# Performance work log

Measured on AMD Instinct MI355X. Metric: run time of the kernel, lower is better.

The kernel has to match this reference:

```python
import jax, jax.numpy as jnp
import numpy as np

B, S, D, H = 2, 2048, 1024, 16
DH = D // H  # key_dim = embed_dim // num_heads
NEG = 1e9    # Keras masked-softmax adder magnitude
EPS = 1e-6


def setup_inputs() -> dict:
    key = jax.random.key(0)
    ks = jax.random.split(key, 6)
    sc = 1.0 / np.sqrt(D)
    return {
        "x": jax.random.normal(ks[0], (B, S, D), jnp.float32),
        "Wq": jax.random.normal(ks[1], (D, H, DH), jnp.float32) * sc,
        "bq": jnp.zeros((H, DH), jnp.float32),
        "Wk": jax.random.normal(ks[2], (D, H, DH), jnp.float32) * sc,
        "bk": jnp.zeros((H, DH), jnp.float32),
        "Wv": jax.random.normal(ks[3], (D, H, DH), jnp.float32) * sc,
        "bv": jnp.zeros((H, DH), jnp.float32),
        "Wo": jax.random.normal(ks[4], (H, DH, D), jnp.float32) * (1.0 / np.sqrt(D)),
        "bo": jnp.zeros((D,), jnp.float32),
        "gamma": jnp.ones((D,), jnp.float32),
        "beta": jnp.zeros((D,), jnp.float32),
    }


def reference(x, Wq, bq, Wk, bk, Wv, bv, Wo, bo, gamma, beta):
    # Keras MultiHeadAttention(query=x, value=x), inference (dropouts are identity)
    q = jnp.einsum("bsd,dhk->bshk", x, Wq) + bq  # [B,S,H,DH]
    k = jnp.einsum("bsd,dhk->bshk", x, Wk) + bk
    v = jnp.einsum("bsd,dhk->bshk", x, Wv) + bv

    scores = jnp.einsum("bqhd,bkhd->bhqk", q, k) / jnp.sqrt(jnp.asarray(DH, x.dtype))
    # Source: mask = 1 - band_part(ones, -1, 0) -> ones strictly ABOVE diagonal.
    # Keras attends where mask==1 and adds (1-mask)*(-1e9) elsewhere. Faithful:
    i = jnp.arange(S)[:, None]
    j = jnp.arange(S)[None, :]
    allowed = (j > i).astype(scores.dtype)  # [S,S], strict upper triangle
    scores = scores + (allowed - 1.0) * NEG  # subtract 1e9 where not allowed
    probs = jax.nn.softmax(scores, axis=-1)

    ctx = jnp.einsum("bhqk,bkhd->bqhd", probs, v)  # [B,S,H,DH]
    attn_out = jnp.einsum("bqhd,hdo->bqo", ctx, Wo) + bo  # [B,S,D]

    # residual + LayerNorm(eps=1e-6)
    y = x + attn_out
    mu = jnp.mean(y, axis=-1, keepdims=True)
    var = jnp.mean(jnp.square(y - mu), axis=-1, keepdims=True)
    return (y - mu) * jax.lax.rsqrt(var + EPS) * gamma + beta
```

## Files before the change

kernel.cpp:

```cpp
#include <hip/hip_runtime.h>
#include <hip/hip_bf16.h>

typedef __hip_bfloat16 bf16;
typedef __attribute__((ext_vector_type(8))) short bf16x8;
typedef __attribute__((ext_vector_type(4))) float f32x4;

constexpr int Bc  = 2;
constexpr int Sc  = 2048;
constexpr int Dc  = 1024;
constexpr int Hc  = 16;
constexpr int DHc = 64;
constexpr int BS  = Bc * Sc;
constexpr int NT  = Sc / 64;

__device__ __forceinline__ float bs2f(unsigned short u) {
    union { unsigned int i; float f; } v; v.i = ((unsigned int)u) << 16; return v.f;
}
__device__ __forceinline__ short f2bs(float x) {
    bf16 h = __float2bfloat16(x);
    return *reinterpret_cast<short*>(&h);
}

typedef const __attribute__((address_space(1))) unsigned int* as1_u32p;
typedef __attribute__((address_space(3))) unsigned int* as3_u32p;
__device__ __forceinline__ void gl_lds16(const void* g, void* l) {
    __builtin_amdgcn_global_load_lds((as1_u32p)g, (as3_u32p)l, 16, 0, 0);
}

__global__ __launch_bounds__(256) void cast_x(const float* __restrict__ in,
                                              short* __restrict__ out) {
    const int i = (blockIdx.x * 256 + threadIdx.x) * 4;
    const float4 v = *(const float4*)(in + i);
    ushort4 o;
    o.x = (unsigned short)f2bs(v.x);
    o.y = (unsigned short)f2bs(v.y);
    o.z = (unsigned short)f2bs(v.z);
    o.w = (unsigned short)f2bs(v.w);
    *(ushort4*)(out + i) = o;
}

__global__ __launch_bounds__(256) void transpose_cast(
    const float* __restrict__ w0, const float* __restrict__ w1,
    const float* __restrict__ w2, const float* __restrict__ w3,
    short* __restrict__ outbase)
{
    __shared__ float T[64][65];
    const int z = blockIdx.z;
    const float* in = (z == 0) ? w0 : (z == 1) ? w1 : (z == 2) ? w2 : w3;
    short* out = outbase + (size_t)z * 1024 * 1024;
    const int k0 = blockIdx.x * 64, n0 = blockIdx.y * 64;
    const int t = threadIdx.x;
    #pragma unroll
    for (int it = 0; it < 4; ++it) {
        const int s = it * 256 + t;
        const int r = s >> 4, c = (s & 15) * 4;
        *(float4*)&T[r][c] = *(const float4*)(in + (size_t)(k0 + r) * 1024 + n0 + c);
    }
    __syncthreads();
    #pragma unroll
    for (int it = 0; it < 4; ++it) {
        const int s = it * 256 + t;
        const int rr = s >> 4, cc = (s & 15) * 4;
        ushort4 o;
        o.x = (unsigned short)f2bs(T[cc + 0][rr]);
        o.y = (unsigned short)f2bs(T[cc + 1][rr]);
        o.z = (unsigned short)f2bs(T[cc + 2][rr]);
        o.w = (unsigned short)f2bs(T[cc + 3][rr]);
        *(ushort4*)(out + (size_t)(n0 + rr) * 1024 + k0 + cc) = o;
    }
}

__global__ __launch_bounds__(256, 3) void gemm_bt(
    const short* __restrict__ A, const short* __restrict__ BTbase,
    const float* __restrict__ b0, const float* __restrict__ b1,
    const float* __restrict__ b2, short* __restrict__ Cbase)
{
    __shared__ __align__(16) short As[128 * 64];
    __shared__ __align__(16) short Bs[128 * 64];

    const int z = blockIdx.z;
    const short* BT = BTbase + (size_t)z * 1024 * 1024;
    const float* bias = (z == 0) ? b0 : (z == 1) ? b1 : b2;
    short* C = Cbase + (size_t)z * BS * Dc;

    const int t = threadIdx.x;
    const int lane = t & 63, w = t >> 6;
    const int quad = lane >> 4, l16 = lane & 15;
    const int wm = (w & 1) * 64, wn = (w >> 1) * 64;
    const int row0 = blockIdx.y * 128;
    const int col0 = blockIdx.x * 128;
    const int sw = l16 & 7;

    f32x4 acc[4][4] = {};

    for (int kt = 0; kt < 1024; kt += 64) {
        __syncthreads();
        #pragma unroll
        for (int i = 0; i < 4; ++i) {
            const int f = i * 256 + t;
            const int r = f >> 3;
            const int g = (f & 7) ^ (r & 7);
            short* lb = &As[(i * 256 + w * 64) * 8];
            gl_lds16(A + (size_t)(row0 + r) * 1024 + kt + g * 8, lb);
            short* lb2 = &Bs[(i * 256 + w * 64) * 8];
            gl_lds16(BT + (size_t)(col0 + r) * 1024 + kt + g * 8, lb2);
        }
        __syncthreads();
        #pragma unroll
        for (int ks = 0; ks < 2; ++ks) {
            bf16x8 av[4], bv[4];
            #pragma unroll
            for (int mt = 0; mt < 4; ++mt) {
                const int r = wm + mt * 16 + l16;
                av[mt] = *(const bf16x8*)&As[r * 64 + ((ks * 4 + quad) ^ sw) * 8];
            }
            #pragma unroll
            for (int nt = 0; nt < 4; ++nt) {
                const int r = wn + nt * 16 + l16;
                bv[nt] = *(const bf16x8*)&Bs[r * 64 + ((ks * 4 + quad) ^ sw) * 8];
            }
            #pragma unroll
            for (int mt = 0; mt < 4; ++mt)
                #pragma unroll
                for (int nt = 0; nt < 4; ++nt)
                    acc[mt][nt] = __builtin_amdgcn_mfma_f32_16x16x32_bf16(
                        av[mt], bv[nt], acc[mt][nt], 0, 0, 0);
        }
    }

    float bvv[4];
    #pragma unroll
    for (int nt = 0; nt < 4; ++nt) bvv[nt] = bias[col0 + wn + nt * 16 + l16];
    #pragma unroll
    for (int mt = 0; mt < 4; ++mt)
        #pragma unroll
        for (int reg = 0; reg < 4; ++reg) {
            const size_t row = row0 + wm + mt * 16 + quad * 4 + reg;
            #pragma unroll
            for (int nt = 0; nt < 4; ++nt) {
                const int col = col0 + wn + nt * 16 + l16;
                C[row * 1024 + col] = f2bs(acc[mt][nt][reg] + bvv[nt]);
            }
        }
}

__device__ __forceinline__ int psw_off(int row, int col) {
    return row * 72 + (row >> 2) * 48 + col;
}

template<bool DIAG>
__device__ __forceinline__ void qtile_step(
    const bf16x8 (&qf)[2],
    const short (&Ks)[64][72], const short (&VsT)[64][72],
    short* __restrict__ Psw,
    const int k0, const int row_base,
    const int quad, const int l16,
    float (&l)[4], f32x4 (&O)[4])
{
    bf16x8 kf[2][4];
    #pragma unroll
    for (int ks = 0; ks < 2; ++ks)
        #pragma unroll
        for (int nt = 0; nt < 4; ++nt)
            kf[ks][nt] = *(const bf16x8*)&Ks[nt * 16 + l16][ks * 32 + quad * 8];

    f32x4 S[4] = {};
    #pragma unroll
    for (int ks = 0; ks < 2; ++ks)
        #pragma unroll
        for (int nt = 0; nt < 4; ++nt)
            S[nt] = __builtin_amdgcn_mfma_f32_16x16x32_bf16(qf[ks], kf[ks][nt], S[nt], 0, 0, 0);

    #pragma unroll
    for (int nt = 0; nt < 4; ++nt) {
        #pragma unroll
        for (int reg = 0; reg < 4; ++reg) {
            float s = fminf(S[nt][reg] * 0.125f, 80.f);
            if (DIAG) {
                const int col = k0 + nt * 16 + l16;
                const int row = row_base + quad * 4 + reg;
                s = (col > row) ? s : -87.0f;
            }
            const float p = __expf(s);
            S[nt][reg] = p;
            l[reg] += p;
        }
    }

    #pragma unroll
    for (int nt = 0; nt < 4; ++nt)
        #pragma unroll
        for (int reg = 0; reg < 4; ++reg)
            Psw[psw_off(quad * 4 + reg, nt * 16 + l16)] = f2bs(S[nt][reg]);

    #pragma unroll
    for (int ks = 0; ks < 2; ++ks) {
        const bf16x8 pf = *(const bf16x8*)&Psw[psw_off(l16, ks * 32 + quad * 8)];
        #pragma unroll
        for (int nt = 0; nt < 4; ++nt) {
            const bf16x8 vf = *(const bf16x8*)&VsT[nt * 16 + l16][ks * 32 + quad * 8];
            O[nt] = __builtin_amdgcn_mfma_f32_16x16x32_bf16(pf, vf, O[nt], 0, 0, 0);
        }
    }
}

__global__ __launch_bounds__(512, 4) void attn_mfma(
    const short* __restrict__ Qg, const short* __restrict__ Kg,
    const short* __restrict__ Vg, short* __restrict__ CTX)
{
    __shared__ __align__(16) short Ks [2][64][72];
    __shared__ __align__(16) short VsT[2][64][72];
    __shared__ __align__(16) short Ps[8][1296];

    const int tid  = threadIdx.x;
    const int lane = tid & 63, w = tid >> 6;
    const int quad = lane >> 4, l16 = lane & 15;
    const int wq   = w & 3;
    const bool isA = (w < 4);
    const int p  = blockIdx.x;
    const int h  = blockIdx.y;
    const int b  = blockIdx.z;
    const size_t rb = (size_t)b * Sc;
    const int cb = h * DHc;

    const int myT0 = isA ? p : (NT - 1 - p);
    const int q0   = myT0 * 64;

    bf16x8 qf[2];
    {
        const short* qp = Qg + (rb + q0 + wq * 16 + l16) * (size_t)Dc + cb + quad * 8;
        qf[0] = *(const bf16x8*)(qp);
        qf[1] = *(const bf16x8*)(qp + 32);
    }

    float l[4] = {};
    f32x4 O[4] = {};

    const int skey = tid & 63, sseg = (tid >> 6) * 8;

    {
        const int buf = p & 1;
        const size_t g = (rb + p * 64 + skey) * (size_t)Dc + cb + sseg;
        const bf16x8 kv = *(const bf16x8*)(Kg + g);
        const bf16x8 vv = *(const bf16x8*)(Vg + g);
        *(bf16x8*)&Ks[buf][skey][sseg] = kv;
        #pragma unroll
        for (int e = 0; e < 8; ++e) VsT[buf][sseg + e][skey] = vv[e];
    }
    __syncthreads();

    for (int t = p; t < NT; ++t) {
        const int cur = t & 1;
        const bool havenext = (t + 1 < NT);
        bf16x8 pk, pv;
        if (havenext) {
            const size_t g = (rb + (t + 1) * 64 + skey) * (size_t)Dc + cb + sseg;
            pk = *(const bf16x8*)(Kg + g);
            pv = *(const bf16x8*)(Vg + g);
        }

        if (t > myT0) {
            qtile_step<false>(qf, Ks[cur], VsT[cur], Ps[w],
                              t * 64, q0 + wq * 16, quad, l16, l, O);
        } else if (t == myT0) {
            qtile_step<true>(qf, Ks[cur], VsT[cur], Ps[w],
                             t * 64, q0 + wq * 16, quad, l16, l, O);
        }

        if (havenext) {
            *(bf16x8*)&Ks[cur ^ 1][skey][sseg] = pk;
            #pragma unroll
            for (int e = 0; e < 8; ++e) VsT[cur ^ 1][sseg + e][skey] = pv[e];
            __syncthreads();
        }
    }

    #pragma unroll
    for (int off = 1; off < 16; off <<= 1)
        #pragma unroll
        for (int reg = 0; reg < 4; ++reg)
            l[reg] += __shfl_xor(l[reg], off, 64);
    #pragma unroll
    for (int reg = 0; reg < 4; ++reg) l[reg] = 1.0f / l[reg];
    #pragma unroll
    for (int nt = 0; nt < 4; ++nt)
        #pragma unroll
        for (int reg = 0; reg < 4; ++reg) {
            const size_t row = rb + q0 + wq * 16 + quad * 4 + reg;
            CTX[row * Dc + cb + nt * 16 + l16] = f2bs(O[nt][reg] * l[reg]);
        }
}

__global__ __launch_bounds__(256) void vmean(const short* __restrict__ V,
                                             short* __restrict__ CTX)
{
    const int h = blockIdx.x, b = blockIdx.y;
    const int t = threadIdx.x;
    const int dh = t & 63, ck = t >> 6;
    float s = 0.f;
    const short* vp = V + ((size_t)b * Sc + ck * 512) * Dc + h * DHc + dh;
    for (int j = 0; j < 512; ++j) s += bs2f(vp[(size_t)j * Dc]);
    __shared__ float red[4][64];
    red[ck][dh] = s;
    __syncthreads();
    if (ck == 0) {
        const float tot = (red[0][dh] + red[1][dh] + red[2][dh] + red[3][dh]) * (1.f / Sc);
        CTX[((size_t)b * Sc + Sc - 1) * Dc + h * DHc + dh] = f2bs(tot);
    }
}

__global__ __launch_bounds__(256, 4) void resid_ln(
    const float* __restrict__ X, const short* __restrict__ AO,
    const float* __restrict__ gamma, const float* __restrict__ beta,
    float* __restrict__ out)
{
    const int r = blockIdx.x;
    const int t = threadIdx.x;
    const size_t base = (size_t)r * Dc + t * 4;

    const float4 x4 = *(const float4*)(X + base);
    const ushort4 a4 = *(const ushort4*)(AO + base);
    float y[4];
    y[0] = x4.x + bs2f(a4.x);
    y[1] = x4.y + bs2f(a4.y);
    y[2] = x4.z + bs2f(a4.z);
    y[3] = x4.w + bs2f(a4.w);

    float s  = y[0] + y[1] + y[2] + y[3];
    float s2 = y[0]*y[0] + y[1]*y[1] + y[2]*y[2] + y[3]*y[3];
    #pragma unroll
    for (int off = 1; off < 64; off <<= 1) {
        s  += __shfl_xor(s,  off, 64);
        s2 += __shfl_xor(s2, off, 64);
    }
    __shared__ float red[8];
    const int w = t >> 6;
    if ((t & 63) == 0) { red[w] = s; red[4 + w] = s2; }
    __syncthreads();
    s  = red[0] + red[1] + red[2] + red[3];
    s2 = red[4] + red[5] + red[6] + red[7];

    const float mu   = s * (1.0f / Dc);
    const float rstd = rsqrtf(s2 * (1.0f / Dc) - mu * mu + 1e-6f);

    const float4 g4 = *(const float4*)(gamma + t * 4);
    const float4 b4 = *(const float4*)(beta  + t * 4);
    float4 o;
    o.x = (y[0] - mu) * rstd * g4.x + b4.x;
    o.y = (y[1] - mu) * rstd * g4.y + b4.y;
    o.z = (y[2] - mu) * rstd * g4.z + b4.z;
    o.w = (y[3] - mu) * rstd * g4.w + b4.w;
    *(float4*)(out + base) = o;
}

extern "C" void kernel_launch(void* const* d_in, const int* in_sizes, int n_in,
                              void* d_out, int out_size, void* d_ws, size_t ws_size,
                              hipStream_t stream)
{
    (void)in_sizes; (void)n_in; (void)out_size; (void)ws_size;
    const float* x     = (const float*)d_in[0];
    const float* Wq    = (const float*)d_in[1];
    const float* bq    = (const float*)d_in[2];
    const float* Wk    = (const float*)d_in[3];
    const float* bk    = (const float*)d_in[4];
    const float* Wv    = (const float*)d_in[5];
    const float* bv    = (const float*)d_in[6];
    const float* Wo    = (const float*)d_in[7];
    const float* bo    = (const float*)d_in[8];
    const float* gamma = (const float*)d_in[9];
    const float* beta  = (const float*)d_in[10];
    float* out = (float*)d_out;

    const size_t matN = (size_t)BS * Dc;
    const size_t wN   = (size_t)Dc * Dc;
    short* xb = (short*)d_ws;
    short* WT = xb + matN;
    short* Qb = WT + 4 * wN;
    short* Kb = Qb + matN;
    short* Vb = Kb + matN;
    short* Cx = Vb + matN;
    short* AO = Qb;

    cast_x<<<matN / 1024, 256, 0, stream>>>(x, xb);

    dim3 gt(16, 16, 4);
    transpose_cast<<<gt, 256, 0, stream>>>(Wq, Wk, Wv, Wo, WT);

    dim3 gq(Dc / 128, BS / 128, 3);
    gemm_bt<<<gq, 256, 0, stream>>>(xb, WT, bq, bk, bv, Qb);

    dim3 ga(16, Hc, Bc);
    attn_mfma<<<ga, 512, 0, stream>>>(Qb, Kb, Vb, Cx);

    dim3 gv(Hc, Bc);
    vmean<<<gv, 256, 0, stream>>>(Vb, Cx);

    dim3 go(Dc / 128, BS / 128, 1);
    gemm_bt<<<go, 256, 0, stream>>>(Cx, WT + 3 * wN, bo, bo, bo, AO);

    resid_ln<<<BS, 256, 0, stream>>>(x, AO, gamma, beta, out);
}
```

Measured before the change: 222.8 us.

## Run attention blocks with 4 waves processing paired query tiles sequentially

New measurement: 221.6 us. Within noise of the previous version (-0.5%).

```diff
diff --git a/kernel.cpp b/kernel.cpp
--- a/kernel.cpp
+++ b/kernel.cpp
@@ -144,15 +144,12 @@
         }
 }
 
-__device__ __forceinline__ int psw_off(int row, int col) {
-    return row * 72 + (row >> 2) * 48 + col;
-}
 
 template<bool DIAG>
 __device__ __forceinline__ void qtile_step(
     const bf16x8 (&qf)[2],
     const short (&Ks)[64][72], const short (&VsT)[64][72],
-    short* __restrict__ Psw,
+    short (&Psw)[16][72],
     const int k0, const int row_base,
     const int quad, const int l16,
     float (&l)[4], f32x4 (&O)[4])
@@ -175,27 +172,31 @@
     for (int nt = 0; nt < 4; ++nt) {
         #pragma unroll
         for (int reg = 0; reg < 4; ++reg) {
-            float s = fminf(S[nt][reg] * 0.125f, 80.f);
+            float s = fminf(S[nt][reg] * 0.18033688f, 115.4f);
             if (DIAG) {
                 const int col = k0 + nt * 16 + l16;
                 const int row = row_base + quad * 4 + reg;
-                s = (col > row) ? s : -87.0f;
-            }
-            const float p = __expf(s);
+                s = (col > row) ? s : -126.0f;
+            }
+            const float p = exp2f(s);
             S[nt][reg] = p;
             l[reg] += p;
         }
     }
 
     #pragma unroll
-    for (int nt = 0; nt < 4; ++nt)
-        #pragma unroll
-        for (int reg = 0; reg < 4; ++reg)
-            Psw[psw_off(quad * 4 + reg, nt * 16 + l16)] = f2bs(S[nt][reg]);
+    for (int reg = 0; reg < 4; ++reg) {
+        const __hip_bfloat162 lo = __float22bfloat162_rn(make_float2(S[0][reg], S[1][reg]));
+        const __hip_bfloat162 hi = __float22bfloat162_rn(make_float2(S[2][reg], S[3][reg]));
+        uint2 u;
+        u.x = *reinterpret_cast<const unsigned int*>(&lo);
+        u.y = *reinterpret_cast<const unsigned int*>(&hi);
+        *(uint2*)&Psw[quad * 4 + reg][l16 * 4] = u;
+    }
 
     #pragma unroll
     for (int ks = 0; ks < 2; ++ks) {
-        const bf16x8 pf = *(const bf16x8*)&Psw[psw_off(l16, ks * 32 + quad * 8)];
+        const bf16x8 pf = *(const bf16x8*)&Psw[l16][ks * 32 + quad * 8];
         #pragma unroll
         for (int nt = 0; nt < 4; ++nt) {
             const bf16x8 vf = *(const bf16x8*)&VsT[nt * 16 + l16][ks * 32 + quad * 8];
@@ -204,91 +205,107 @@
     }
 }
 
-__global__ __launch_bounds__(512, 4) void attn_mfma(
+__global__ __launch_bounds__(256, 3) void attn_mfma(
     const short* __restrict__ Qg, const short* __restrict__ Kg,
     const short* __restrict__ Vg, short* __restrict__ CTX)
 {
     __shared__ __align__(16) short Ks [2][64][72];
     __shared__ __align__(16) short VsT[2][64][72];
-    __shared__ __align__(16) short Ps[8][1296];
+    __shared__ __align__(16) short Ps[4][16][72];
 
     const int tid  = threadIdx.x;
     const int lane = tid & 63, w = tid >> 6;
     const int quad = lane >> 4, l16 = lane & 15;
-    const int wq   = w & 3;
-    const bool isA = (w < 4);
     const int p  = blockIdx.x;
     const int h  = blockIdx.y;
     const int b  = blockIdx.z;
     const size_t rb = (size_t)b * Sc;
     const int cb = h * DHc;
 
-    const int myT0 = isA ? p : (NT - 1 - p);
-    const int q0   = myT0 * 64;
-
-    bf16x8 qf[2];
-    {
-        const short* qp = Qg + (rb + q0 + wq * 16 + l16) * (size_t)Dc + cb + quad * 8;
-        qf[0] = *(const bf16x8*)(qp);
-        qf[1] = *(const bf16x8*)(qp + 32);
-    }
-
-    float l[4] = {};
-    f32x4 O[4] = {};
-
     const int skey = tid & 63, sseg = (tid >> 6) * 8;
-
-    {
-        const int buf = p & 1;
-        const size_t g = (rb + p * 64 + skey) * (size_t)Dc + cb + sseg;
-        const bf16x8 kv = *(const bf16x8*)(Kg + g);
-        const bf16x8 vv = *(const bf16x8*)(Vg + g);
-        *(bf16x8*)&Ks[buf][skey][sseg] = kv;
-        #pragma unroll
-        for (int e = 0; e < 8; ++e) VsT[buf][sseg + e][skey] = vv[e];
-    }
-    __syncthreads();
-
-    for (int t = p; t < NT; ++t) {
-        const int cur = t & 1;
-        const bool havenext = (t + 1 < NT);
-        bf16x8 pk, pv;
-        if (havenext) {
-            const size_t g = (rb + (t + 1) * 64 + skey) * (size_t)Dc + cb + sseg;
-            pk = *(const bf16x8*)(Kg + g);
-            pv = *(const bf16x8*)(Vg + g);
-        }
-
-        if (t > myT0) {
-            qtile_step<false>(qf, Ks[cur], VsT[cur], Ps[w],
-                              t * 64, q0 + wq * 16, quad, l16, l, O);
-        } else if (t == myT0) {
-            qtile_step<true>(qf, Ks[cur], VsT[cur], Ps[w],
-                             t * 64, q0 + wq * 16, quad, l16, l, O);
-        }
-
-        if (havenext) {
-            *(bf16x8*)&Ks[cur ^ 1][skey][sseg] = pk;
-            #pragma unroll
-            for (int e = 0; e < 8; ++e) VsT[cur ^ 1][sseg + e][skey] = pv[e];
-            __syncthreads();
-        }
-    }
-
-    #pragma unroll
-    for (int off = 1; off < 16; off <<= 1)
-        #pragma unroll
-        for (int reg = 0; reg < 4; ++reg)
-            l[reg] += __shfl_xor(l[reg], off, 64);
-    #pragma unroll
-    for (int reg = 0; reg < 4; ++reg) l[reg] = 1.0f / l[reg];
-    #pragma unroll
-    for (int nt = 0; nt < 4; ++nt)
-        #pragma unroll
-        for (int reg = 0; reg < 4; ++reg) {
-            const size_t row = rb + q0 + wq * 16 + quad * 4 + reg;
-            CTX[row * Dc + cb + nt * 16 + l16] = f2bs(O[nt][reg] * l[reg]);
-        }
+    const int pkey = ((skey & 15) << 2) | (skey >> 4);
+
+    #pragma unroll 1
+    for (int ph = 0; ph < 2; ++ph) {
+        const int myq = ph ? (NT - 1 - p) : p;
+        const int t0  = myq;
+        const int q0  = myq * 64;
+
+        bf16x8 qf[2];
+        {
+            const short* qp = Qg + (rb + q0 + w * 16 + l16) * (size_t)Dc + cb + quad * 8;
+            qf[0] = *(const bf16x8*)(qp);
+            qf[1] = *(const bf16x8*)(qp + 32);
+        }
+        float l[4] = {};
+        f32x4 O[4] = {};
+
+        if (ph) __syncthreads();
+
+        {
+            const int buf = t0 & 1;
+            const size_t g = (rb + t0 * 64 + skey) * (size_t)Dc + cb + sseg;
+            const bf16x8 k0v = *(const bf16x8*)(Kg + g);
+            const bf16x8 k1v = *(const bf16x8*)(Kg + g + 32);
+            const bf16x8 v0v = *(const bf16x8*)(Vg + g);
+            const bf16x8 v1v = *(const bf16x8*)(Vg + g + 32);
+            *(bf16x8*)&Ks[buf][skey][sseg]      = k0v;
+            *(bf16x8*)&Ks[buf][skey][sseg + 32] = k1v;
+            #pragma unroll
+            for (int e = 0; e < 8; ++e) {
+                VsT[buf][sseg + e][pkey]      = v0v[e];
+                VsT[buf][sseg + 32 + e][pkey] = v1v[e];
+            }
+        }
+        __syncthreads();
+
+        for (int t = t0; t < NT; ++t) {
+            const int cur = t & 1;
+            const bool havenext = (t + 1 < NT);
+            bf16x8 pk0, pk1, pv0, pv1;
+            if (havenext) {
+                const size_t g = (rb + (t + 1) * 64 + skey) * (size_t)Dc + cb + sseg;
+                pk0 = *(const bf16x8*)(Kg + g);
+                pk1 = *(const bf16x8*)(Kg + g + 32);
+                pv0 = *(const bf16x8*)(Vg + g);
+                pv1 = *(const bf16x8*)(Vg + g + 32);
+            }
+
+            if (t == t0)
+                qtile_step<true >(qf, Ks[cur], VsT[cur], Ps[w],
+                                  t * 64, q0 + w * 16, quad, l16, l, O);
+            else
+                qtile_step<false>(qf, Ks[cur], VsT[cur], Ps[w],
+                                  t * 64, q0 + w * 16, quad, l16, l, O);
+
+            if (havenext) {
+                const int nb = cur ^ 1;
+                *(bf16x8*)&Ks[nb][skey][sseg]      = pk0;
+                *(bf16x8*)&Ks[nb][skey][sseg + 32] = pk1;
+                #pragma unroll
+                for (int e = 0; e < 8; ++e) {
+                    VsT[nb][sseg + e][pkey]      = pv0[e];
+                    VsT[nb][sseg + 32 + e][pkey] = pv1[e];
+                }
+                __syncthreads();
+            }
+        }
+
+        #pragma unroll
+        for (int off = 1; off < 16; off <<= 1)
+            #pragma unroll
+            for (int reg = 0; reg < 4; ++reg)
+                l[reg] += __shfl_xor(l[reg], off, 64);
+        #pragma unroll
+        for (int reg = 0; reg < 4; ++reg) l[reg] = 1.0f / l[reg];
+        #pragma unroll
+        for (int nt = 0; nt < 4; ++nt)
+            #pragma unroll
+            for (int reg = 0; reg < 4; ++reg) {
+                const size_t row = rb + q0 + w * 16 + quad * 4 + reg;
+                CTX[row * Dc + cb + nt * 16 + l16] = f2bs(O[nt][reg] * l[reg]);
+            }
+    }
 }
 
 __global__ __launch_bounds__(256) void vmean(const short* __restrict__ V,
@@ -390,7 +407,7 @@
     gemm_bt<<<gq, 256, 0, stream>>>(xb, WT, bq, bk, bv, Qb);
 
     dim3 ga(16, Hc, Bc);
-    attn_mfma<<<ga, 512, 0, stream>>>(Qb, Kb, Vb, Cx);
+    attn_mfma<<<ga, 256, 0, stream>>>(Qb, Kb, Vb, Cx);
 
     dim3 gv(Hc, Bc);
     vmean<<<gv, 256, 0, stream>>>(Vb, Cx);
```
